# Performance work log

Hardware: AMD Instinct MI355X
Metric: run time of the kernel (lower is better)

Reference implementation:

```python
import jax, jax.numpy as jnp
import numpy as np

PH = PW = 5  # roi_size
EPS = 1e-5


def _conv1x1(x, w, b):
    # x: (B,Cin,H,W), w: (Cout,Cin)
    return jnp.einsum('bchw,oc->bohw', x, w) + b[None, :, None, None]


def _resize_ac(x, oh, ow):
    # F.interpolate bilinear, align_corners=True. x: (B,C,H,W)
    B, C, H, W = x.shape
    ys = jnp.linspace(0.0, H - 1.0, oh)
    xs = jnp.linspace(0.0, W - 1.0, ow)
    y0 = jnp.floor(ys).astype(jnp.int32); y1 = jnp.minimum(y0 + 1, H - 1)
    x0 = jnp.floor(xs).astype(jnp.int32); x1 = jnp.minimum(x0 + 1, W - 1)
    ly = (ys - y0)[:, None]; lx = (xs - x0)[None, :]
    v00 = x[:, :, y0[:, None], x0[None, :]]
    v01 = x[:, :, y0[:, None], x1[None, :]]
    v10 = x[:, :, y1[:, None], x0[None, :]]
    v11 = x[:, :, y1[:, None], x1[None, :]]
    return v00 * (1 - ly) * (1 - lx) + v01 * (1 - ly) * lx + v10 * ly * (1 - lx) + v11 * ly * lx


def _roi_align_one(feat, box):
    # torchvision RoIAlign, spatial_scale=1, sampling_ratio=1, aligned=False
    # feat: (C,H,W), box: (x1,y1,x2,y2)
    C, H, W = feat.shape
    bx1, by1, bx2, by2 = box[0], box[1], box[2], box[3]
    rw = jnp.maximum(bx2 - bx1, 1.0)
    rh = jnp.maximum(by2 - by1, 1.0)
    xs = bx1 + (jnp.arange(PW, dtype=feat.dtype) + 0.5) * (rw / PW)
    ys = by1 + (jnp.arange(PH, dtype=feat.dtype) + 0.5) * (rh / PH)
    yg = jnp.broadcast_to(ys[:, None], (PH, PW))
    xg = jnp.broadcast_to(xs[None, :], (PH, PW))
    valid = (yg >= -1.0) & (yg <= H) & (xg >= -1.0) & (xg <= W)
    y = jnp.clip(yg, 0.0, H - 1.0); x = jnp.clip(xg, 0.0, W - 1.0)
    y0 = jnp.floor(y).astype(jnp.int32); x0 = jnp.floor(x).astype(jnp.int32)
    y1i = jnp.minimum(y0 + 1, H - 1); x1i = jnp.minimum(x0 + 1, W - 1)
    ly = y - y0; lx = x - x0
    v = (feat[:, y0, x0] * (1 - ly) * (1 - lx) + feat[:, y0, x1i] * (1 - ly) * lx
         + feat[:, y1i, x0] * ly * (1 - lx) + feat[:, y1i, x1i] * ly * lx)
    return v * valid  # (C,PH,PW)


def _layernorm(x, w, b):
    mu = jnp.mean(x, -1, keepdims=True)
    var = jnp.var(x, -1, keepdims=True)
    return (x - mu) * jax.lax.rsqrt(var + EPS) * w + b


def setup_inputs() -> dict:
    key = jax.random.key(0)
    ks = jax.random.split(key, 16)
    B, G, NB, HF = 8, 8, 16, 28
    x4 = jax.random.normal(ks[0], (B, 1024, 14, 14), jnp.float32)
    x5 = jax.random.normal(ks[1], (B, 2048, 7, 7), jnp.float32)
    bx = jax.random.uniform(ks[2], (B, NB), minval=0.0, maxval=18.0)
    by = jax.random.uniform(ks[3], (B, NB), minval=0.0, maxval=18.0)
    bw = jax.random.uniform(ks[4], (B, NB), minval=3.0, maxval=10.0)
    bh = jax.random.uniform(ks[5], (B, NB), minval=3.0, maxval=10.0)
    boxes = jnp.stack([bx, by, jnp.minimum(bx + bw, 28.0), jnp.minimum(by + bh, 28.0)], -1)
    group = jax.random.randint(ks[6], (B, G, 2), 0, NB, jnp.int32)
    real_in_num = jnp.full((B,), G, jnp.int32)
    label_s = jax.random.randint(ks[7], (B, G), 0, 6, jnp.int64)
    label_s = jnp.where(jnp.arange(G)[None, :] % 3 == 0, -1, label_s)  # exercise both branches
    skeleton = jax.random.normal(ks[8], (B, G, HF, HF), jnp.float32)
    D = 1536 * PH * PW  # 38400
    return {
        'x4': x4, 'x5': x5, 'boxes': boxes, 'skeleton': skeleton,
        'group': group, 'real_in_num': real_in_num, 'label_s': label_s,
        'conv1_w': jax.random.normal(ks[9], (), jnp.float32) * 0.5,
        'conv1_b': jax.random.normal(ks[10], (), jnp.float32) * 0.1,
        'conv2_w': jax.random.normal(ks[11], (512, 1024), jnp.float32) * 0.03,
        'conv2_b': jnp.zeros((512,), jnp.float32),
        'conv3_w': jax.random.normal(ks[12], (1024, 2048), jnp.float32) * 0.02,
        'conv3_b': jnp.zeros((1024,), jnp.float32),
        'norm1_w': jnp.ones((D,), jnp.float32), 'norm1_b': jnp.zeros((D,), jnp.float32),
        'norm2_w': jnp.ones((512,), jnp.float32), 'norm2_b': jnp.zeros((512,), jnp.float32),
        'fc1_w': jax.random.normal(ks[13], (512, D), jnp.float32) * float(np.sqrt(2.0 / D)),
        'fc1_b': jnp.zeros((512,), jnp.float32),
        'fc2_w': jax.random.normal(ks[14], (6, 512), jnp.float32) * float(np.sqrt(2.0 / 512)),
        'fc2_b': jnp.zeros((6,), jnp.float32),
    }


def reference(x4, x5, boxes, skeleton, group, real_in_num, label_s,
              conv1_w, conv1_b, conv2_w, conv2_b, conv3_w, conv3_b,
              norm1_w, norm1_b, norm2_w, norm2_b, fc1_w, fc1_b, fc2_w, fc2_b):
    B, G = skeleton.shape[0], skeleton.shape[1]
    HF, WF = skeleton.shape[2], skeleton.shape[3]
    # backbone heads: 1x1 conv + bilinear upsample (align_corners=True), concat
    f4 = _resize_ac(_conv1x1(x4, conv2_w, conv2_b), HF, WF)   # (B,512,28,28)
    f5 = _resize_ac(_conv1x1(x5, conv3_w, conv3_b), HF, WF)   # (B,1024,28,28)
    app = jnp.concatenate([f4, f5], axis=1)                   # (B,1536,28,28)
    C = app.shape[1]
    # per-person pose gate: 1x1 conv (scalar on single channel) + sigmoid
    gate = jax.nn.sigmoid(skeleton * conv1_w + conv1_b)       # (B,G,28,28)
    gated = gate[:, :, None] * app[:, None]                   # (B,G,C,28,28)
    use_gate = (label_s != -1)[:, :, None, None, None]
    pose_feature = jnp.where(use_gate, gated, app[:, None])   # (B,G,C,28,28)
    # union box of the two interacting people (get_box_tensor)
    bidx = jnp.arange(B)[:, None]
    b1 = boxes[bidx, group[..., 0]]                           # (B,G,4)
    b2 = boxes[bidx, group[..., 1]]
    ub = jnp.stack([jnp.minimum(b1[..., 0], b2[..., 0]), jnp.minimum(b1[..., 1], b2[..., 1]),
                    jnp.maximum(b1[..., 2], b2[..., 2]), jnp.maximum(b1[..., 3], b2[..., 3])], -1)
    # batched RoIAlign over all N = B*G boxes
    feats = pose_feature.reshape(B * G, C, HF, WF)
    rois = jax.vmap(_roi_align_one)(feats, ub.reshape(B * G, 4))  # (N,C,5,5)
    sk = rois.reshape(B * G, -1)                              # (N,38400)
    sk = jax.nn.relu(_layernorm(sk, norm1_w, norm1_b))
    # dropout(p=0.9) is identity in eval mode
    sk = sk @ fc1_w.T + fc1_b
    sk = _layernorm(sk, norm2_w, norm2_b)
    score = sk @ fc2_w.T + fc2_b                              # (N,6)
    return score
```

## Files before the change

### kernel.cpp

```cpp
#include <hip/hip_runtime.h>
#include <math.h>

#define B8   8
#define HW4  196
#define HW5  49
#define HFW  28
#define NPIX 784
#define CAPP 1536
#define D1   38400
#define NR   64
#define NSP  100

typedef short short8 __attribute__((ext_vector_type(8)));
typedef short short4v __attribute__((ext_vector_type(4)));
typedef float floatx16 __attribute__((ext_vector_type(16)));

__device__ __forceinline__ unsigned short f2bf(float f) {
  unsigned u = __float_as_uint(f);
  u += 0x7FFF + ((u >> 16) & 1);
  return (unsigned short)(u >> 16);
}

struct Params {
  const float *x4, *x5, *boxes, *skel;
  const int *group, *label;
  const float *c1w, *c1b, *w2c, *b2c, *w3c, *b3c;
  const float *n1w, *n1b, *n2w, *n2b, *fw1, *fb1, *fw2, *fb2;
  float* out;
  unsigned short *x4T, *x5T, *sknT;
  float *f4T, *f5T, *tap4w, *tap5w, *descw, *roisP, *stats, *fc1P, *out1;
  int *tap4o, *tap5o, *desco;
};

union SharedU {
  float tile[32 * 201];
  struct {
    unsigned short As[2][4096];
    unsigned short Bs[2][4096];
  } g;
  struct {
    float cw4[16], cw5[16], wgs;
    int co4[16], co5[16];
    float red[8];
  } roi;
  struct {
    float red[8];
    float red2[24];
  } ln;
};

__device__ __forceinline__ void gemm_unit(
    SharedU& sh, const unsigned short* __restrict__ A, const float* __restrict__ Bw,
    float* __restrict__ C, int mt, int nt, int k0, int kchunk,
    int K, int N, int Mvalid, bool accum) {
  int t = threadIdx.x;
  int wave = t >> 6, lane = t & 63;
  int wm = wave & 1, wn = wave >> 1;
  const unsigned short* Aptr = A + (size_t)(mt * 64) * K + k0;
  const float* Bptr = Bw + (size_t)(nt * 64) * K + k0;
  short8 areg[2];
  float4 breg[4];
  floatx16 acc;
#pragma unroll
  for (int i = 0; i < 16; i++) acc[i] = 0.f;
  int nkb = kchunk >> 6;

#pragma unroll
  for (int i = 0; i < 2; i++) {
    int e = t + i * 256;
    areg[i] = *(const short8*)(Aptr + (size_t)(e >> 3) * K + (e & 7) * 8);
  }
#pragma unroll
  for (int i = 0; i < 4; i++) {
    int e = t + i * 256;
    breg[i] = *(const float4*)(Bptr + (size_t)(e >> 4) * K + (e & 15) * 4);
  }
#pragma unroll
  for (int i = 0; i < 2; i++) {
    int e = t + i * 256;
    int m = e >> 3, ko = e & 7;
    *(short8*)&sh.g.As[0][ko * 512 + ((m ^ ko)) * 8] = areg[i];
  }
#pragma unroll
  for (int i = 0; i < 4; i++) {
    int e = t + i * 256;
    short4v v;
    v[0] = (short)f2bf(breg[i].x); v[1] = (short)f2bf(breg[i].y);
    v[2] = (short)f2bf(breg[i].z); v[3] = (short)f2bf(breg[i].w);
    int ko = (e & 15) >> 1, half = (e & 15) & 1, n = e >> 4;
    *(short4v*)&sh.g.Bs[0][ko * 512 + ((n ^ ko)) * 8 + half * 4] = v;
  }
  __syncthreads();

  for (int kb = 0; kb < nkb; kb++) {
    int buf = kb & 1;
    bool more = (kb + 1) < nkb;
    if (more) {
      int kof = (kb + 1) * 64;
#pragma unroll
      for (int i = 0; i < 2; i++) {
        int e = t + i * 256;
        areg[i] = *(const short8*)(Aptr + (size_t)(e >> 3) * K + kof + (e & 7) * 8);
      }
#pragma unroll
      for (int i = 0; i < 4; i++) {
        int e = t + i * 256;
        breg[i] = *(const float4*)(Bptr + (size_t)(e >> 4) * K + kof + (e & 15) * 4);
      }
    }
#pragma unroll
    for (int s = 0; s < 4; s++) {
      int ko = 2 * s + (lane >> 5);
      int am = wm * 32 + (lane & 31);
      int bn = wn * 32 + (lane & 31);
      short8 af = *(const short8*)&sh.g.As[buf][ko * 512 + ((am ^ ko)) * 8];
      short8 bf = *(const short8*)&sh.g.Bs[buf][ko * 512 + ((bn ^ ko)) * 8];
      acc = __builtin_amdgcn_mfma_f32_32x32x16_bf16(af, bf, acc, 0, 0, 0);
    }
    __syncthreads();
    if (more) {
      int nb2 = 1 - buf;
#pragma unroll
      for (int i = 0; i < 2; i++) {
        int e = t + i * 256;
        int m = e >> 3, ko = e & 7;
        *(short8*)&sh.g.As[nb2][ko * 512 + ((m ^ ko)) * 8] = areg[i];
      }
#pragma unroll
      for (int i = 0; i < 4; i++) {
        int e = t + i * 256;
        short4v v;
        v[0] = (short)f2bf(breg[i].x); v[1] = (short)f2bf(breg[i].y);
        v[2] = (short)f2bf(breg[i].z); v[3] = (short)f2bf(breg[i].w);
        int ko = (e & 15) >> 1, half = (e & 15) & 1, n = e >> 4;
        *(short4v*)&sh.g.Bs[nb2][ko * 512 + ((n ^ ko)) * 8 + half * 4] = v;
      }
      __syncthreads();
    }
  }

  int col = nt * 64 + wn * 32 + (lane & 31);
  int rbase = mt * 64 + wm * 32 + 4 * (lane >> 5);
  if (accum) {
#pragma unroll
    for (int reg = 0; reg < 16; reg++) {
      int row = rbase + (reg & 3) + 8 * (reg >> 2);
      if (row < Mvalid) atomicAdd(&C[(size_t)row * N + col], acc[reg]);
    }
  } else {
#pragma unroll
    for (int reg = 0; reg < 16; reg++) {
      int row = rbase + (reg & 3) + 8 * (reg >> 2);
      if (row < Mvalid) C[(size_t)row * N + col] = acc[reg];
    }
  }
}

__device__ __forceinline__ float gate_val(const float* sk, int yy, int xx,
                                          float c1w, float c1b, bool use) {
  if (!use) return 1.f;
  float z = sk[yy * HFW + xx] * c1w + c1b;
  return 1.f / (1.f + expf(-z));
}

__device__ void run_phase0(const Params& p, SharedU& sh) {
  int bid = blockIdx.x, t = threadIdx.x, gb = gridDim.x;
  int gtid = bid * 256 + t;
  int nth = gb * 256;
  float4 z4 = make_float4(0.f, 0.f, 0.f, 0.f);
  for (int i = gtid; i < 319488; i += nth) ((float4*)p.f4T)[i] = z4;
  if (gtid < 128) p.stats[gtid] = 0.f;

  for (int u = bid; u < 836; u += gb) {
    __syncthreads();
    if (u < 256) {
      int b = u >> 5, cc = u & 31;
      for (int i = t; i < 32 * HW4; i += 256) {
        int c = i / HW4, hw = i - c * HW4;
        sh.tile[c * 201 + hw] = p.x4[((size_t)(b * 1024 + cc * 32 + c)) * HW4 + hw];
      }
      __syncthreads();
      for (int i = t; i < HW4 * 32; i += 256) {
        int hw = i >> 5, c = i & 31;
        p.x4T[((size_t)(b * HW4 + hw)) * 1024 + cc * 32 + c] = f2bf(sh.tile[c * 201 + hw]);
      }
    } else if (u < 768) {
      int u2 = u - 256;
      int b = u2 >> 6, cc = u2 & 63;
      for (int i = t; i < 32 * HW5; i += 256) {
        int c = i / HW5, hw = i - c * HW5;
        sh.tile[c * 51 + hw] = p.x5[((size_t)(b * 2048 + cc * 32 + c)) * HW5 + hw];
      }
      __syncthreads();
      for (int i = t; i < HW5 * 32; i += 256) {
        int hw = i >> 5, c = i & 31;
        p.x5T[((size_t)(b * HW5 + hw)) * 2048 + cc * 32 + c] = f2bf(sh.tile[c * 51 + hw]);
      }
    } else if (u < 832) {
      int bg = u - 768;
      if (t < 25) {
        int b = bg >> 3;
        int i1 = p.group[bg * 2 + 0], i2 = p.group[bg * 2 + 1];
        const float* bb1 = p.boxes + (size_t)(b * 16 + i1) * 4;
        const float* bb2 = p.boxes + (size_t)(b * 16 + i2) * 4;
        float ux1 = fminf(bb1[0], bb2[0]);
        float uy1 = fminf(bb1[1], bb2[1]);
        float ux2 = fmaxf(bb1[2], bb2[2]);
        float uy2 = fmaxf(bb1[3], bb2[3]);
        float rw = fmaxf(ux2 - ux1, 1.0f), rh = fmaxf(uy2 - uy1, 1.0f);
        int iy = t / 5, ix = t % 5;
        float sy = uy1 + (iy + 0.5f) * (rh * 0.2f);
        float sx = ux1 + (ix + 0.5f) * (rw * 0.2f);
        float valid = (sy >= -1.0f && sy <= 28.0f && sx >= -1.0f && sx <= 28.0f) ? 1.f : 0.f;
        float y = fminf(fmaxf(sy, 0.f), 27.f);
        float x = fminf(fmaxf(sx, 0.f), 27.f);
        int y0 = (int)floorf(y), x0 = (int)floorf(x);
        int y1 = min(y0 + 1, 27), x1 = min(x0 + 1, 27);
        float ly = y - (float)y0, lx = x - (float)x0;
        bool use = (p.label[bg] != -1);
        float c1w = p.c1w[0], c1b = p.c1b[0];
        const float* sk = p.skel + (size_t)bg * NPIX;
        int idx = (bg * 25 + t) * 4;
        p.descw[idx + 0] = (1.f - ly) * (1.f - lx) * valid * gate_val(sk, y0, x0, c1w, c1b, use);
        p.descw[idx + 1] = (1.f - ly) * lx * valid * gate_val(sk, y0, x1, c1w, c1b, use);
        p.descw[idx + 2] = ly * (1.f - lx) * valid * gate_val(sk, y1, x0, c1w, c1b, use);
        p.descw[idx + 3] = ly * lx * valid * gate_val(sk, y1, x1, c1w, c1b, use);
        p.desco[idx + 0] = y0 * HFW + x0;
        p.desco[idx + 1] = y0 * HFW + x1;
        p.desco[idx + 2] = y1 * HFW + x0;
        p.desco[idx + 3] = y1 * HFW + x1;
      }
    } else {
      int pix = (u - 832) * 196 + t;
      if (t < 196) {
        int y = pix / HFW, x = pix % HFW;
        {
          float sy = y * (13.0f / 27.0f), sx = x * (13.0f / 27.0f);
          int y0 = (int)sy, x0 = (int)sx;
          int y1 = min(y0 + 1, 13), x1 = min(x0 + 1, 13);
          float ly = sy - y0, lx = sx - x0;
          p.tap4o[pix * 4 + 0] = y0 * 14 + x0; p.tap4w[pix * 4 + 0] = (1.f - ly) * (1.f - lx);
          p.tap4o[pix * 4 + 1] = y0 * 14 + x1; p.tap4w[pix * 4 + 1] = (1.f - ly) * lx;
          p.tap4o[pix * 4 + 2] = y1 * 14 + x0; p.tap4w[pix * 4 + 2] = ly * (1.f - lx);
          p.tap4o[pix * 4 + 3] = y1 * 14 + x1; p.tap4w[pix * 4 + 3] = ly * lx;
        }
        {
          float sy = y * (6.0f / 27.0f), sx = x * (6.0f / 27.0f);
          int y0 = (int)sy, x0 = (int)sx;
          int y1 = min(y0 + 1, 6), x1 = min(x0 + 1, 6);
          float ly = sy - y0, lx = sx - x0;
          p.tap5o[pix * 4 + 0] = y0 * 7 + x0; p.tap5w[pix * 4 + 0] = (1.f - ly) * (1.f - lx);
          p.tap5o[pix * 4 + 1] = y0 * 7 + x1; p.tap5w[pix * 4 + 1] = (1.f - ly) * lx;
          p.tap5o[pix * 4 + 2] = y1 * 7 + x0; p.tap5w[pix * 4 + 2] = ly * (1.f - lx);
          p.tap5o[pix * 4 + 3] = y1 * 7 + x1; p.tap5w[pix * 4 + 3] = ly * lx;
        }
      }
    }
  }
}

__device__ void run_phase1(const Params& p, SharedU& sh) {
  int bid = blockIdx.x, gb = gridDim.x;
  for (int u = bid; u < 1696; u += gb) {
    __syncthreads();
    if (u < 800) {
      int mt = u % 25, r = u / 25;
      int nt = r & 7, sp = r >> 3;
      gemm_unit(sh, p.x4T, p.w2c, p.f4T, mt, nt, sp * 256, 256, 1024, 512, 1568, true);
    } else {
      int u2 = u - 800;
      int mt = u2 % 7, r = u2 / 7;
      int nt = r & 15, sp = r >> 4;
      gemm_unit(sh, p.x5T, p.w3c, p.f5T, mt, nt, sp * 256, 256, 2048, 1024, 392, true);
    }
  }
}

__device__ void run_phase2(const Params& p, SharedU& sh) {
  int bid = blockIdx.x, t = threadIdx.x, gb = gridDim.x;
  for (int u = bid; u < 1600; u += gb) {
    __syncthreads();
    int pp = u % 25, bg = u / 25, b = bg >> 3;
    int di = (bg * 25 + pp) * 4;
    if (t < 16) {
      int i = t >> 2, j = t & 3;
      float wg = p.descw[di + i];
      int pix = p.desco[di + i];
      sh.roi.cw4[t] = wg * p.tap4w[pix * 4 + j];
      sh.roi.co4[t] = (b * HW4 + p.tap4o[pix * 4 + j]) * 512;
      sh.roi.cw5[t] = wg * p.tap5w[pix * 4 + j];
      sh.roi.co5[t] = (b * HW5 + p.tap5o[pix * 4 + j]) * 1024;
    }
    if (t == 16) sh.roi.wgs = p.descw[di] + p.descw[di + 1] + p.descw[di + 2] + p.descw[di + 3];
    __syncthreads();
    float w4r[16], w5r[16];
    int o4r[16], o5r[16];
    float wg = sh.roi.wgs;
#pragma unroll
    for (int i = 0; i < 16; i++) {
      w4r[i] = sh.roi.cw4[i]; o4r[i] = sh.roi.co4[i];
      w5r[i] = sh.roi.cw5[i]; o5r[i] = sh.roi.co5[i];
    }
    float ls = 0.f, ls2 = 0.f;
    float* outp = p.roisP + (size_t)(bg * 25 + pp) * CAPP;
    for (int c = t; c < 512; c += 256) {
      float acc = wg * p.b2c[c];
#pragma unroll
      for (int i = 0; i < 16; i++) acc = fmaf(w4r[i], p.f4T[o4r[i] + c], acc);
      outp[c] = acc;
      ls += acc; ls2 = fmaf(acc, acc, ls2);
    }
    for (int c = t; c < 1024; c += 256) {
      float acc = wg * p.b3c[c];
#pragma unroll
      for (int i = 0; i < 16; i++) acc = fmaf(w5r[i], p.f5T[o5r[i] + c], acc);
      outp[512 + c] = acc;
      ls += acc; ls2 = fmaf(acc, acc, ls2);
    }
    for (int off = 32; off; off >>= 1) {
      ls += __shfl_down(ls, off);
      ls2 += __shfl_down(ls2, off);
    }
    int wv = t >> 6;
    if ((t & 63) == 0) { sh.roi.red[wv] = ls; sh.roi.red[4 + wv] = ls2; }
    __syncthreads();
    if (t == 0) {
      atomicAdd(&p.stats[bg * 2 + 0], sh.roi.red[0] + sh.roi.red[1] + sh.roi.red[2] + sh.roi.red[3]);
      atomicAdd(&p.stats[bg * 2 + 1], sh.roi.red[4] + sh.roi.red[5] + sh.roi.red[6] + sh.roi.red[7]);
    }
  }
}

__device__ void run_phase3(const Params& p, SharedU& sh) {
  int bid = blockIdx.x, t = threadIdx.x, gb = gridDim.x;
  for (int u = bid; u < 384; u += gb) {
    __syncthreads();
    int r = u / 6, ch = u - r * 6;
    int c0 = ch * 256;
    float S = p.stats[r * 2], S2 = p.stats[r * 2 + 1];
    float mu = S * (1.f / D1);
    float var = S2 * (1.f / D1) - mu * mu;
    float rs = rsqrtf(var + 1e-5f);
    const float* rp = p.roisP + (size_t)r * 25 * CAPP + c0;
#pragma unroll
    for (int pp = 0; pp < 25; pp++)
      sh.tile[pp * 257 + t] = rp[(size_t)pp * CAPP + t];
    __syncthreads();
    unsigned short* op = p.sknT + (size_t)r * D1 + c0 * 25;
    const float* wv = p.n1w + c0 * 25;
    const float* bv = p.n1b + c0 * 25;
    for (int j = t; j < 6400; j += 256) {
      unsigned cc = (unsigned)j / 25u;
      unsigned pp = (unsigned)j - cc * 25u;
      float x = sh.tile[pp * 257 + cc];
      float v = fmaf((x - mu) * rs, wv[j], bv[j]);
      op[j] = f2bf(fmaxf(v, 0.f));
    }
  }
}

__device__ void run_phase4(const Params& p, SharedU& sh) {
  int bid = blockIdx.x, gb = gridDim.x;
  for (int u = bid; u < 8 * NSP; u += gb) {
    __syncthreads();
    int nt = u & 7, sp = u >> 3;
    gemm_unit(sh, p.sknT, p.fw1, p.fc1P + (size_t)sp * (NR * 512),
              0, nt, sp * 384, 384, 38400, 512, 64, false);
  }
}

__device__ void run_phase5a(const Params& p, SharedU& sh) {
  int bid = blockIdx.x, t = threadIdx.x;
  int r = bid >> 3, cb = bid & 7;
  int c = cb * 64 + (t & 63), sg = t >> 6;
  const float* pq = p.fc1P + (size_t)r * 512 + c;
  float v = 0.f;
#pragma unroll 5
  for (int s = sg * 25; s < sg * 25 + 25; s++)
    v += pq[(size_t)s * (NR * 512)];
  sh.tile[sg * 64 + (t & 63)] = v;
  __syncthreads();
  if (t < 64) {
    float r0 = sh.tile[t] + sh.tile[64 + t] + sh.tile[128 + t] + sh.tile[192 + t];
    p.out1[(size_t)r * 512 + cb * 64 + t] = r0 + p.fb1[cb * 64 + t];
  }
}

__device__ void run_phase5b(const Params& p, SharedU& sh) {
  int bid = blockIdx.x, t = threadIdx.x, gb = gridDim.x;
  for (int r = bid; r < NR; r += gb) {
    __syncthreads();
    int j1 = t, j2 = t + 256;
    float v1 = p.out1[r * 512 + j1];
    float v2 = p.out1[r * 512 + j2];
    float s = v1 + v2, s2 = v1 * v1 + v2 * v2;
    for (int off = 32; off; off >>= 1) {
      s += __shfl_down(s, off);
      s2 += __shfl_down(s2, off);
    }
    int wv = t >> 6;
    if ((t & 63) == 0) { sh.ln.red[wv] = s; sh.ln.red[4 + wv] = s2; }
    __syncthreads();
    float S = sh.ln.red[0] + sh.ln.red[1] + sh.ln.red[2] + sh.ln.red[3];
    float S2 = sh.ln.red[4] + sh.ln.red[5] + sh.ln.red[6] + sh.ln.red[7];
    float mu = S / 512.f;
    float var = S2 / 512.f - mu * mu;
    float rs = rsqrtf(var + 1e-5f);
    float n1v = fmaf((v1 - mu) * rs, p.n2w[j1], p.n2b[j1]);
    float n2v = fmaf((v2 - mu) * rs, p.n2w[j2], p.n2b[j2]);
    float pm[6];
#pragma unroll
    for (int m = 0; m < 6; m++)
      pm[m] = n1v * p.fw2[m * 512 + j1] + n2v * p.fw2[m * 512 + j2];
#pragma unroll
    for (int m = 0; m < 6; m++)
      for (int off = 32; off; off >>= 1) pm[m] += __shfl_down(pm[m], off);
    if ((t & 63) == 0) {
#pragma unroll
      for (int m = 0; m < 6; m++) sh.ln.red2[wv * 6 + m] = pm[m];
    }
    __syncthreads();
    if (t < 6)
      p.out[r * 6 + t] = sh.ln.red2[t] + sh.ln.red2[6 + t] + sh.ln.red2[12 + t] +
                         sh.ln.red2[18 + t] + p.fb2[t];
  }
}

__global__ __launch_bounds__(256, 4) void k_phase0(Params p) { __shared__ SharedU sh; run_phase0(p, sh); }
__global__ __launch_bounds__(256, 4) void k_phase1(Params p) { __shared__ SharedU sh; run_phase1(p, sh); }
__global__ __launch_bounds__(256, 4) void k_phase2(Params p) { __shared__ SharedU sh; run_phase2(p, sh); }
__global__ __launch_bounds__(256, 4) void k_phase3(Params p) { __shared__ SharedU sh; run_phase3(p, sh); }
__global__ __launch_bounds__(256, 4) void k_phase4(Params p) { __shared__ SharedU sh; run_phase4(p, sh); }
__global__ __launch_bounds__(256, 4) void k_phase5a(Params p) { __shared__ SharedU sh; run_phase5a(p, sh); }
__global__ __launch_bounds__(256, 4) void k_phase5b(Params p) { __shared__ SharedU sh; run_phase5b(p, sh); }

extern "C" void kernel_launch(void* const* d_in, const int* in_sizes, int n_in,
                              void* d_out, int out_size, void* d_ws, size_t ws_size,
                              hipStream_t stream) {
  Params p;
  p.x4    = (const float*)d_in[0];
  p.x5    = (const float*)d_in[1];
  p.boxes = (const float*)d_in[2];
  p.skel  = (const float*)d_in[3];
  p.group = (const int*)d_in[4];
  p.label = (const int*)d_in[6];
  p.c1w   = (const float*)d_in[7];
  p.c1b   = (const float*)d_in[8];
  p.w2c   = (const float*)d_in[9];
  p.b2c   = (const float*)d_in[10];
  p.w3c   = (const float*)d_in[11];
  p.b3c   = (const float*)d_in[12];
  p.n1w   = (const float*)d_in[13];
  p.n1b   = (const float*)d_in[14];
  p.n2w   = (const float*)d_in[15];
  p.n2b   = (const float*)d_in[16];
  p.fw1   = (const float*)d_in[17];
  p.fb1   = (const float*)d_in[18];
  p.fw2   = (const float*)d_in[19];
  p.fb2   = (const float*)d_in[20];
  p.out   = (float*)d_out;

  float* ws = (float*)d_ws;
  p.x4T   = (unsigned short*)ws;
  p.x5T   = (unsigned short*)(ws + 819200);
  p.f4T   = ws + 1277952;
  p.f5T   = ws + 2097152;
  p.tap4w = ws + 2555904;
  p.tap4o = (int*)(ws + 2559040);
  p.tap5w = ws + 2562176;
  p.tap5o = (int*)(ws + 2565312);
  p.descw = ws + 2568448;
  p.desco = (int*)(ws + 2574848);
  p.roisP = ws + 2581248;
  p.stats = ws + 5038848;
  p.sknT  = (unsigned short*)(ws + 5038976);
  p.fc1P  = ws + 6267776;
  p.out1  = ws + 9544576;

  k_phase0<<<836,  256, 0, stream>>>(p);
  k_phase1<<<1696, 256, 0, stream>>>(p);
  k_phase2<<<1600, 256, 0, stream>>>(p);
  k_phase3<<<384,  256, 0, stream>>>(p);
  k_phase4<<<800,  256, 0, stream>>>(p);
  k_phase5a<<<512, 256, 0, stream>>>(p);
  k_phase5b<<<64,  256, 0, stream>>>(p);
}
```

Baseline: 256.0 us.

## Replace split-K partial buffer with atomic accumulation and deepen GEMM prefetch

The fc1 split-K GEMM now accumulates directly into a zero-initialised output with atomicAdd instead of writing 100 partial slabs and reducing them in a separate kernel, which removes one launch and a large partial-sum round trip through memory. The split count changes from 100 to 120 chunks of 320 K. The GEMM inner loop now prefetches two stages ahead in registers and needs only one barrier per K step. Costs include atomic contention (120 adds per output element), nondeterministic summation order, and higher register use.

```diff
diff --git a/kernel.cpp b/kernel.cpp
--- a/kernel.cpp
+++ b/kernel.cpp
@@ -9,7 +9,6 @@
 #define CAPP 1536
 #define D1   38400
 #define NR   64
-#define NSP  100
 
 typedef short short8 __attribute__((ext_vector_type(8)));
 typedef short short4v __attribute__((ext_vector_type(4)));
@@ -28,7 +27,7 @@
   const float *n1w, *n1b, *n2w, *n2b, *fw1, *fb1, *fw2, *fb2;
   float* out;
   unsigned short *x4T, *x5T, *sknT;
-  float *f4T, *f5T, *tap4w, *tap5w, *descw, *roisP, *stats, *fc1P, *out1;
+  float *f4T, *f5T, *tap4w, *tap5w, *descw, *roisP, *stats, *out1;
   int *tap4o, *tap5o, *desco;
 };
 
@@ -58,56 +57,46 @@
   int wm = wave & 1, wn = wave >> 1;
   const unsigned short* Aptr = A + (size_t)(mt * 64) * K + k0;
   const float* Bptr = Bw + (size_t)(nt * 64) * K + k0;
-  short8 areg[2];
-  float4 breg[4];
+
+  int m0 = t >> 3, ka = (t & 7) * 8, koa = t & 7;
+  int n0 = t >> 4, kbo = (t & 15) * 4, kob = (t & 15) >> 1, half = t & 1;
+
+  short8 areg[2][2];
+  float4 breg[2][4];
   floatx16 acc;
 #pragma unroll
   for (int i = 0; i < 16; i++) acc[i] = 0.f;
   int nkb = kchunk >> 6;
 
-#pragma unroll
-  for (int i = 0; i < 2; i++) {
-    int e = t + i * 256;
-    areg[i] = *(const short8*)(Aptr + (size_t)(e >> 3) * K + (e & 7) * 8);
-  }
-#pragma unroll
-  for (int i = 0; i < 4; i++) {
-    int e = t + i * 256;
-    breg[i] = *(const float4*)(Bptr + (size_t)(e >> 4) * K + (e & 15) * 4);
-  }
-#pragma unroll
-  for (int i = 0; i < 2; i++) {
-    int e = t + i * 256;
-    int m = e >> 3, ko = e & 7;
-    *(short8*)&sh.g.As[0][ko * 512 + ((m ^ ko)) * 8] = areg[i];
-  }
-#pragma unroll
-  for (int i = 0; i < 4; i++) {
-    int e = t + i * 256;
-    short4v v;
-    v[0] = (short)f2bf(breg[i].x); v[1] = (short)f2bf(breg[i].y);
-    v[2] = (short)f2bf(breg[i].z); v[3] = (short)f2bf(breg[i].w);
-    int ko = (e & 15) >> 1, half = (e & 15) & 1, n = e >> 4;
-    *(short4v*)&sh.g.Bs[0][ko * 512 + ((n ^ ko)) * 8 + half * 4] = v;
-  }
+  auto LOAD = [&](int s, int j) {
+    int kof = j * 64;
+    areg[s][0] = *(const short8*)(Aptr + (size_t)m0 * K + kof + ka);
+    areg[s][1] = *(const short8*)(Aptr + (size_t)(m0 + 32) * K + kof + ka);
+#pragma unroll
+    for (int i = 0; i < 4; i++)
+      breg[s][i] = *(const float4*)(Bptr + (size_t)(n0 + 16 * i) * K + kof + kbo);
+  };
+  auto STORE = [&](int buf, int s) {
+    *(short8*)&sh.g.As[buf][koa * 512 + ((m0 ^ koa)) * 8] = areg[s][0];
+    *(short8*)&sh.g.As[buf][koa * 512 + (((m0 + 32) ^ koa)) * 8] = areg[s][1];
+#pragma unroll
+    for (int i = 0; i < 4; i++) {
+      short4v v;
+      v[0] = (short)f2bf(breg[s][i].x); v[1] = (short)f2bf(breg[s][i].y);
+      v[2] = (short)f2bf(breg[s][i].z); v[3] = (short)f2bf(breg[s][i].w);
+      int n = n0 + 16 * i;
+      *(short4v*)&sh.g.Bs[buf][kob * 512 + ((n ^ kob)) * 8 + half * 4] = v;
+    }
+  };
+
+  LOAD(0, 0);
+  STORE(0, 0);
+  if (nkb > 1) LOAD(1, 1);
   __syncthreads();
 
   for (int kb = 0; kb < nkb; kb++) {
     int buf = kb & 1;
-    bool more = (kb + 1) < nkb;
-    if (more) {
-      int kof = (kb + 1) * 64;
-#pragma unroll
-      for (int i = 0; i < 2; i++) {
-        int e = t + i * 256;
-        areg[i] = *(const short8*)(Aptr + (size_t)(e >> 3) * K + kof + (e & 7) * 8);
-      }
-#pragma unroll
-      for (int i = 0; i < 4; i++) {
-        int e = t + i * 256;
-        breg[i] = *(const float4*)(Bptr + (size_t)(e >> 4) * K + kof + (e & 15) * 4);
-      }
-    }
+    if (kb + 2 < nkb) LOAD(buf, kb + 2);
 #pragma unroll
     for (int s = 0; s < 4; s++) {
       int ko = 2 * s + (lane >> 5);
@@ -117,26 +106,8 @@
       short8 bf = *(const short8*)&sh.g.Bs[buf][ko * 512 + ((bn ^ ko)) * 8];
       acc = __builtin_amdgcn_mfma_f32_32x32x16_bf16(af, bf, acc, 0, 0, 0);
     }
-    __syncthreads();
-    if (more) {
-      int nb2 = 1 - buf;
-#pragma unroll
-      for (int i = 0; i < 2; i++) {
-        int e = t + i * 256;
-        int m = e >> 3, ko = e & 7;
-        *(short8*)&sh.g.As[nb2][ko * 512 + ((m ^ ko)) * 8] = areg[i];
-      }
-#pragma unroll
-      for (int i = 0; i < 4; i++) {
-        int e = t + i * 256;
-        short4v v;
-        v[0] = (short)f2bf(breg[i].x); v[1] = (short)f2bf(breg[i].y);
-        v[2] = (short)f2bf(breg[i].z); v[3] = (short)f2bf(breg[i].w);
-        int ko = (e & 15) >> 1, half = (e & 15) & 1, n = e >> 4;
-        *(short4v*)&sh.g.Bs[nb2][ko * 512 + ((n ^ ko)) * 8 + half * 4] = v;
-      }
-      __syncthreads();
-    }
+    if (kb + 1 < nkb) STORE(1 - buf, (kb + 1) & 1);
+    __syncthreads();
   }
 
   int col = nt * 64 + wn * 32 + (lane & 31);
@@ -169,6 +140,7 @@
   int nth = gb * 256;
   float4 z4 = make_float4(0.f, 0.f, 0.f, 0.f);
   for (int i = gtid; i < 319488; i += nth) ((float4*)p.f4T)[i] = z4;
+  for (int i = gtid; i < 8192; i += nth) ((float4*)p.out1)[i] = z4;
   if (gtid < 128) p.stats[gtid] = 0.f;
 
   for (int u = bid; u < 836; u += gb) {
@@ -361,38 +333,20 @@
 
 __device__ void run_phase4(const Params& p, SharedU& sh) {
   int bid = blockIdx.x, gb = gridDim.x;
-  for (int u = bid; u < 8 * NSP; u += gb) {
+  for (int u = bid; u < 960; u += gb) {
     __syncthreads();
     int nt = u & 7, sp = u >> 3;
-    gemm_unit(sh, p.sknT, p.fw1, p.fc1P + (size_t)sp * (NR * 512),
-              0, nt, sp * 384, 384, 38400, 512, 64, false);
-  }
-}
-
-__device__ void run_phase5a(const Params& p, SharedU& sh) {
-  int bid = blockIdx.x, t = threadIdx.x;
-  int r = bid >> 3, cb = bid & 7;
-  int c = cb * 64 + (t & 63), sg = t >> 6;
-  const float* pq = p.fc1P + (size_t)r * 512 + c;
-  float v = 0.f;
-#pragma unroll 5
-  for (int s = sg * 25; s < sg * 25 + 25; s++)
-    v += pq[(size_t)s * (NR * 512)];
-  sh.tile[sg * 64 + (t & 63)] = v;
-  __syncthreads();
-  if (t < 64) {
-    float r0 = sh.tile[t] + sh.tile[64 + t] + sh.tile[128 + t] + sh.tile[192 + t];
-    p.out1[(size_t)r * 512 + cb * 64 + t] = r0 + p.fb1[cb * 64 + t];
-  }
-}
-
-__device__ void run_phase5b(const Params& p, SharedU& sh) {
+    gemm_unit(sh, p.sknT, p.fw1, p.out1, 0, nt, sp * 320, 320, 38400, 512, 64, true);
+  }
+}
+
+__device__ void run_phase5(const Params& p, SharedU& sh) {
   int bid = blockIdx.x, t = threadIdx.x, gb = gridDim.x;
   for (int r = bid; r < NR; r += gb) {
     __syncthreads();
     int j1 = t, j2 = t + 256;
-    float v1 = p.out1[r * 512 + j1];
-    float v2 = p.out1[r * 512 + j2];
+    float v1 = p.out1[r * 512 + j1] + p.fb1[j1];
+    float v2 = p.out1[r * 512 + j2] + p.fb1[j2];
     float s = v1 + v2, s2 = v1 * v1 + v2 * v2;
     for (int off = 32; off; off >>= 1) {
       s += __shfl_down(s, off);
@@ -431,8 +385,7 @@
 __global__ __launch_bounds__(256, 4) void k_phase2(Params p) { __shared__ SharedU sh; run_phase2(p, sh); }
 __global__ __launch_bounds__(256, 4) void k_phase3(Params p) { __shared__ SharedU sh; run_phase3(p, sh); }
 __global__ __launch_bounds__(256, 4) void k_phase4(Params p) { __shared__ SharedU sh; run_phase4(p, sh); }
-__global__ __launch_bounds__(256, 4) void k_phase5a(Params p) { __shared__ SharedU sh; run_phase5a(p, sh); }
-__global__ __launch_bounds__(256, 4) void k_phase5b(Params p) { __shared__ SharedU sh; run_phase5b(p, sh); }
+__global__ __launch_bounds__(256, 4) void k_phase5(Params p) { __shared__ SharedU sh; run_phase5(p, sh); }
 
 extern "C" void kernel_launch(void* const* d_in, const int* in_sizes, int n_in,
                               void* d_out, int out_size, void* d_ws, size_t ws_size,
@@ -474,14 +427,12 @@
   p.roisP = ws + 2581248;
   p.stats = ws + 5038848;
   p.sknT  = (unsigned short*)(ws + 5038976);
-  p.fc1P  = ws + 6267776;
-  p.out1  = ws + 9544576;
+  p.out1  = ws + 6267776;
 
   k_phase0<<<836,  256, 0, stream>>>(p);
   k_phase1<<<1696, 256, 0, stream>>>(p);
   k_phase2<<<1600, 256, 0, stream>>>(p);
   k_phase3<<<384,  256, 0, stream>>>(p);
-  k_phase4<<<800,  256, 0, stream>>>(p);
-  k_phase5a<<<512, 256, 0, stream>>>(p);
-  k_phase5b<<<64,  256, 0, stream>>>(p);
-}
+  k_phase4<<<960,  256, 0, stream>>>(p);
+  k_phase5<<<64,   256, 0, stream>>>(p);
+}
```

New measurement: 249.6 us. -2.5%, faster.
